# Kernel optimization log

Hardware: AMD Instinct MI355X
Metric: run time of the kernel (lower is better)

The kernel has to match this reference:

```python
import jax, jax.numpy as jnp
import numpy as np

C = 64
C8 = C // 8
C16 = C // 16


def setup_inputs() -> dict:
    key = jax.random.key(0)
    ks = jax.random.split(key, 11)
    s = lambda fan_in: 1.0 / np.sqrt(fan_in)
    return {
        "x": jax.random.normal(ks[0], (4, C, 64, 64), dtype=jnp.float32),
        # 1x1 convs == per-pixel linear: weight [out, in], bias [out]
        "Wq": jax.random.uniform(ks[1], (C8, C), minval=-s(C), maxval=s(C)),
        "bq": jax.random.uniform(ks[2], (C8,), minval=-s(C), maxval=s(C)),
        "Wk": jax.random.uniform(ks[3], (C8, C), minval=-s(C), maxval=s(C)),
        "bk": jax.random.uniform(ks[4], (C8,), minval=-s(C), maxval=s(C)),
        "Wv": jax.random.uniform(ks[5], (C, C), minval=-s(C), maxval=s(C)),
        "bv": jax.random.uniform(ks[6], (C,), minval=-s(C), maxval=s(C)),
        "W1": jax.random.uniform(ks[7], (C16, C), minval=-s(C), maxval=s(C)),
        "b1": jax.random.uniform(ks[8], (C16,), minval=-s(C), maxval=s(C)),
        "W2": jax.random.uniform(ks[9], (C, C16), minval=-s(C16), maxval=s(C16)),
        "b2": jax.random.uniform(ks[10], (C,), minval=-s(C16), maxval=s(C16)),
    }


def reference(x, Wq, bq, Wk, bk, Wv, bv, W1, b1, W2, b2):
    b, c, h, w = x.shape
    n = h * w
    xf = x.reshape(b, c, n)                                   # [b,c,n]
    Q = jnp.einsum('qc,bcn->bnq', Wq, xf) + bq                # [b,n,c/8]
    K = jnp.einsum('kc,bcn->bkn', Wk, xf) + bk[None, :, None] # [b,c/8,n]
    V = jnp.einsum('vc,bcn->bvn', Wv, xf) + bv[None, :, None] # [b,c,n]
    scores = jnp.einsum('bnq,bqm->bnm', Q, K) / jnp.sqrt(jnp.float32(c))
    att = jax.nn.softmax(scores, axis=-1)                     # [b,n,n]
    # self_attention_map = V @ att^T
    sa = jnp.einsum('bvm,bnm->bvn', V, att).reshape(b, c, h, w)
    # SE-style channel gate
    avg = xf.mean(axis=2)                                     # [b,c]
    gate = jax.nn.sigmoid(jax.nn.relu(avg @ W1.T + b1) @ W2.T + b2)
    return sa * gate[:, :, None, None]
```

## Files before the change

kernel.cpp:

```cpp
#include <hip/hip_runtime.h>
#include <hip/hip_bf16.h>

typedef __attribute__((ext_vector_type(8))) short bf16x8;
typedef __attribute__((ext_vector_type(4))) float f32x4;
typedef __attribute__((ext_vector_type(4))) unsigned short u16x4;
typedef __attribute__((ext_vector_type(8))) unsigned short u16x8;

#define WS_QB 0
#define WS_KB 131072
#define WS_VB 262144
#define WS_AVG_U 1310720

__device__ __forceinline__ unsigned short bf_hi(float x) {
    __hip_bfloat16 h = __float2bfloat16(x);
    return *reinterpret_cast<unsigned short*>(&h);
}

__global__ __launch_bounds__(256) void proj_kernel(
    const float* __restrict__ x,
    const float* __restrict__ Wq, const float* __restrict__ bq,
    const float* __restrict__ Wk, const float* __restrict__ bk,
    const float* __restrict__ Wv, const float* __restrict__ bv,
    unsigned short* __restrict__ Qb, unsigned short* __restrict__ Kb,
    unsigned short* __restrict__ Vb, float* __restrict__ avg)
{
    __shared__ __align__(16) unsigned short Wls[80 * 72];

    const int t = threadIdx.x;
    const int w = t >> 6;
    const int l = t & 63;
    const int g = l >> 4;
    const int l15 = l & 15;
    const int b = blockIdx.x >> 6;
    const int n0 = (blockIdx.x & 63) << 6;
    const int n = n0 + w * 16 + l15;
    const float* xb = x + b * 262144;

    float xr[2][8];
#pragma unroll
    for (int kcb = 0; kcb < 2; ++kcb)
#pragma unroll
        for (int j = 0; j < 8; ++j)
            xr[kcb][j] = xb[(kcb * 32 + g * 8 + j) * 4096 + n];

#pragma unroll
    for (int i = 0; i < 20; ++i) {
        const int idx = i * 256 + t;
        const int row = idx >> 6, col = idx & 63;
        float wv;
        if (row < 8)       wv = Wq[row * 64 + col];
        else if (row < 16) wv = Wk[(row - 8) * 64 + col];
        else               wv = Wv[(row - 16) * 64 + col];
        Wls[row * 72 + col] = bf_hi(wv);
    }
    __syncthreads();

    bf16x8 bfr[2];
#pragma unroll
    for (int kcb = 0; kcb < 2; ++kcb)
#pragma unroll
        for (int j = 0; j < 8; ++j)
            bfr[kcb][j] = (short)bf_hi(xr[kcb][j]);

#pragma unroll
    for (int tile = 0; tile < 5; ++tile) {
        const bf16x8 a0 = *(const bf16x8*)&Wls[(tile * 16 + l15) * 72 + g * 8];
        const bf16x8 a1 = *(const bf16x8*)&Wls[(tile * 16 + l15) * 72 + 32 + g * 8];
        f32x4 acc;
#pragma unroll
        for (int r = 0; r < 4; ++r) acc[r] = 0.0f;
        acc = __builtin_amdgcn_mfma_f32_16x16x32_bf16(a0, bfr[0], acc, 0, 0, 0);
        acc = __builtin_amdgcn_mfma_f32_16x16x32_bf16(a1, bfr[1], acc, 0, 0, 0);

        if (tile == 0) {
            u16x4 ov;
            if (g < 2) {
#pragma unroll
                for (int r = 0; r < 4; ++r) ov[r] = bf_hi((acc[r] + bq[g * 4 + r]) * 0.125f);
                *(u16x4*)&Qb[(b * 4096 + n) * 8 + g * 4] = ov;
            } else {
#pragma unroll
                for (int r = 0; r < 4; ++r) ov[r] = bf_hi(acc[r] + bk[(g - 2) * 4 + r]);
                *(u16x4*)&Kb[(b * 4096 + n) * 8 + (g - 2) * 4] = ov;
            }
        } else {
#pragma unroll
            for (int r = 0; r < 4; ++r) {
                const int v = (tile - 1) * 16 + g * 4 + r;
                Vb[(b * 64 + v) * 4096 + n] = bf_hi(acc[r] + bv[v]);
            }
        }
    }

    {
        const int c = t >> 2;
        const float* xrow = xb + c * 4096 + n0 + ((t & 3) << 4);
        float s = 0.0f;
#pragma unroll
        for (int k = 0; k < 4; ++k) {
            const float4 v = *(const float4*)&xrow[k * 4];
            s += (v.x + v.y) + (v.z + v.w);
        }
        s += __shfl_xor(s, 1);
        s += __shfl_xor(s, 2);
        if ((t & 3) == 0) atomicAdd(&avg[b * 64 + c], s * (1.0f / 4096.0f));
    }
}

__global__ __launch_bounds__(256) void attn_kernel(
    const unsigned short* __restrict__ Qb, const unsigned short* __restrict__ Kb,
    const unsigned short* __restrict__ Vb, const float* __restrict__ avg,
    const float* __restrict__ W1, const float* __restrict__ b1,
    const float* __restrict__ W2, const float* __restrict__ b2,
    float* __restrict__ out)
{
    __shared__ __align__(16) unsigned short Vs[2][64][64];
    __shared__ __align__(16) unsigned short Ps[32][64];
    __shared__ float zls[32], gls[64], avgs[64];

    const int t = threadIdx.x;
    const int w = t >> 6;
    const int l = t & 63;
    const int g = l >> 4;
    const int l15 = l & 15;

    const int wg = (blockIdx.x & 7) * 64 + (blockIdx.x >> 3);
    const int b = wg >> 7;
    const int q0 = (wg & 127) << 5;

    if (t < 32) zls[t] = 0.0f;
    if (t < 64) avgs[t] = avg[b * 64 + t];

    bf16x8 zf = {};
    bf16x8 qf[2];
#pragma unroll
    for (int qt = 0; qt < 2; ++qt) {
        bf16x8 v = *(const bf16x8*)&Qb[(b * 4096 + q0 + qt * 16 + l15) * 8];
        qf[qt] = (g == 0) ? v : zf;
    }

    const int srow = t >> 2;
    const int scol = (t & 3) << 4;
    const int ssw = (srow & 7) << 3;
    const unsigned short* vsrc = &Vb[(b * 64 + srow) * 4096];

    {
        u16x8 a = *(const u16x8*)&vsrc[scol];
        u16x8 c = *(const u16x8*)&vsrc[scol + 8];
        *(u16x8*)&Vs[0][srow][scol ^ ssw] = a;
        *(u16x8*)&Vs[0][srow][(scol + 8) ^ ssw] = c;
    }
    const int mrow = w * 16 + l15;
    bf16x8 kf_next;
    {
        bf16x8 kv = *(const bf16x8*)&Kb[(b * 4096 + mrow) * 8];
        kf_next = (g == 0) ? kv : zf;
    }

    f32x4 acc[2];
#pragma unroll
    for (int qt = 0; qt < 2; ++qt)
#pragma unroll
        for (int r = 0; r < 4; ++r) acc[qt][r] = 0.0f;
    float zreg[2] = {0.f, 0.f};
    const int vsw = (l15 & 7) << 3;
    const int psw = (l15 & 7) << 3;

    for (int i = 0; i < 64; ++i) {
        __syncthreads();

        const int inx = (i < 63) ? i + 1 : 63;
        u16x8 va = *(const u16x8*)&vsrc[inx * 64 + scol];
        u16x8 vb2 = *(const u16x8*)&vsrc[inx * 64 + scol + 8];

        bf16x8 kf = kf_next;
        {
            bf16x8 kv = *(const bf16x8*)&Kb[(b * 4096 + inx * 64 + mrow) * 8];
            kf_next = (g == 0) ? kv : zf;
        }
        f32x4 dz;
#pragma unroll
        for (int r = 0; r < 4; ++r) dz[r] = 0.0f;
#pragma unroll
        for (int qt = 0; qt < 2; ++qt) {
            f32x4 d = __builtin_amdgcn_mfma_f32_16x16x32_bf16(kf, qf[qt], dz, 0, 0, 0);
            float p[4];
#pragma unroll
            for (int r = 0; r < 4; ++r) p[r] = __expf(d[r]);
            zreg[qt] += (p[0] + p[1]) + (p[2] + p[3]);
            u16x4 pw;
#pragma unroll
            for (int r = 0; r < 4; ++r) pw[r] = bf_hi(p[r]);
            const int q = qt * 16 + l15;
            *(u16x4*)&Ps[q][(w * 16 + g * 4) ^ ((q & 7) << 3)] = pw;
        }

        __syncthreads();

        {
            unsigned short* dst = &Vs[(i + 1) & 1][srow][0];
            *(u16x8*)&dst[scol ^ ssw] = va;
            *(u16x8*)&dst[(scol + 8) ^ ssw] = vb2;
        }

        {
            const unsigned short* vbuf = &Vs[i & 1][w * 16 + l15][0];
#pragma unroll
            for (int kcb = 0; kcb < 2; ++kcb) {
                const int colA = kcb * 32 + g * 8;
                const bf16x8 af = *(const bf16x8*)&vbuf[colA ^ vsw];
#pragma unroll
                for (int qt = 0; qt < 2; ++qt) {
                    const bf16x8 bfr = *(const bf16x8*)&Ps[qt * 16 + l15][colA ^ psw];
                    acc[qt] = __builtin_amdgcn_mfma_f32_16x16x32_bf16(af, bfr, acc[qt], 0, 0, 0);
                }
            }
        }
    }

#pragma unroll
    for (int qt = 0; qt < 2; ++qt) {
        float z = zreg[qt];
        z += __shfl_xor(z, 16);
        z += __shfl_xor(z, 32);
        if (g == 0) atomicAdd(&zls[qt * 16 + l15], z);
    }
    if (t < 64) {
        float hreg[4];
#pragma unroll
        for (int j = 0; j < 4; ++j) {
            float hh = b1[j];
            for (int c = 0; c < 64; ++c) hh += W1[j * 64 + c] * avgs[c];
            hreg[j] = fmaxf(hh, 0.0f);
        }
        float gg = b2[t];
#pragma unroll
        for (int j = 0; j < 4; ++j) gg += W2[t * 4 + j] * hreg[j];
        gls[t] = 1.0f / (1.0f + __expf(-gg));
    }
    __syncthreads();

#pragma unroll
    for (int qt = 0; qt < 2; ++qt) {
        const int q = qt * 16 + l15;
        const float rz = 1.0f / zls[q];
#pragma unroll
        for (int r = 0; r < 4; ++r) {
            const int v = w * 16 + g * 4 + r;
            out[(b * 64 + v) * 4096 + q0 + q] = acc[qt][r] * rz * gls[v];
        }
    }
}

extern "C" void kernel_launch(void* const* d_in, const int* in_sizes, int n_in,
                              void* d_out, int out_size, void* d_ws, size_t ws_size,
                              hipStream_t stream) {
    const float* x  = (const float*)d_in[0];
    const float* Wq = (const float*)d_in[1];
    const float* bq = (const float*)d_in[2];
    const float* Wk = (const float*)d_in[3];
    const float* bk = (const float*)d_in[4];
    const float* Wv = (const float*)d_in[5];
    const float* bv = (const float*)d_in[6];
    const float* W1 = (const float*)d_in[7];
    const float* b1 = (const float*)d_in[8];
    const float* W2 = (const float*)d_in[9];
    const float* b2 = (const float*)d_in[10];

    unsigned short* wsu = (unsigned short*)d_ws;
    unsigned short* Qb = wsu + WS_QB;
    unsigned short* Kb = wsu + WS_KB;
    unsigned short* Vb = wsu + WS_VB;
    float* avg = (float*)(wsu + WS_AVG_U);
    float* out = (float*)d_out;

    hipMemsetAsync(avg, 0, 256 * sizeof(float), stream);
    proj_kernel<<<256, 256, 0, stream>>>(x, Wq, bq, Wk, bk, Wv, bv, Qb, Kb, Vb, avg);
    attn_kernel<<<512, 256, 0, stream>>>(Qb, Kb, Vb, avg, W1, b1, W2, b2, out);
}
```

Measured before the change: 123.2 us.

## Split projection across output tiles and single-barrier double-buffer attention loop

The projection kernel now launches five times as many blocks, each computing one 16-row output tile (Q/K or a V slice). This raises parallelism but reloads x five times. The attention loop double-buffers the P scratch as well as V, which lets it drop one of the two barriers per iteration. It also raises wave priority around the MFMA section with s_setprio.

```diff
diff --git a/kernel.cpp b/kernel.cpp
--- a/kernel.cpp
+++ b/kernel.cpp
@@ -24,15 +24,18 @@
     unsigned short* __restrict__ Qb, unsigned short* __restrict__ Kb,
     unsigned short* __restrict__ Vb, float* __restrict__ avg)
 {
-    __shared__ __align__(16) unsigned short Wls[80 * 72];
-
-    const int t = threadIdx.x;
-    const int w = t >> 6;
-    const int l = t & 63;
+    __shared__ __align__(16) unsigned short Wls[16 * 72];
+
+    const int tid = threadIdx.x;
+    const int w = tid >> 6;
+    const int l = tid & 63;
     const int g = l >> 4;
     const int l15 = l & 15;
-    const int b = blockIdx.x >> 6;
-    const int n0 = (blockIdx.x & 63) << 6;
+
+    const int tile = blockIdx.x >> 8;
+    const int pair = blockIdx.x & 255;
+    const int b = pair >> 6;
+    const int n0 = (pair & 63) << 6;
     const int n = n0 + w * 16 + l15;
     const float* xb = x + b * 262144;
 
@@ -44,13 +47,12 @@
             xr[kcb][j] = xb[(kcb * 32 + g * 8 + j) * 4096 + n];
 
 #pragma unroll
-    for (int i = 0; i < 20; ++i) {
-        const int idx = i * 256 + t;
+    for (int i = 0; i < 4; ++i) {
+        const int idx = i * 256 + tid;
         const int row = idx >> 6, col = idx & 63;
         float wv;
-        if (row < 8)       wv = Wq[row * 64 + col];
-        else if (row < 16) wv = Wk[(row - 8) * 64 + col];
-        else               wv = Wv[(row - 16) * 64 + col];
+        if (tile == 0) wv = (row < 8) ? Wq[row * 64 + col] : Wk[(row - 8) * 64 + col];
+        else           wv = Wv[((tile - 1) * 16 + row) * 64 + col];
         Wls[row * 72 + col] = bf_hi(wv);
     }
     __syncthreads();
@@ -62,39 +64,27 @@
         for (int j = 0; j < 8; ++j)
             bfr[kcb][j] = (short)bf_hi(xr[kcb][j]);
 
-#pragma unroll
-    for (int tile = 0; tile < 5; ++tile) {
-        const bf16x8 a0 = *(const bf16x8*)&Wls[(tile * 16 + l15) * 72 + g * 8];
-        const bf16x8 a1 = *(const bf16x8*)&Wls[(tile * 16 + l15) * 72 + 32 + g * 8];
-        f32x4 acc;
-#pragma unroll
-        for (int r = 0; r < 4; ++r) acc[r] = 0.0f;
-        acc = __builtin_amdgcn_mfma_f32_16x16x32_bf16(a0, bfr[0], acc, 0, 0, 0);
-        acc = __builtin_amdgcn_mfma_f32_16x16x32_bf16(a1, bfr[1], acc, 0, 0, 0);
-
-        if (tile == 0) {
-            u16x4 ov;
-            if (g < 2) {
-#pragma unroll
-                for (int r = 0; r < 4; ++r) ov[r] = bf_hi((acc[r] + bq[g * 4 + r]) * 0.125f);
-                *(u16x4*)&Qb[(b * 4096 + n) * 8 + g * 4] = ov;
-            } else {
-#pragma unroll
-                for (int r = 0; r < 4; ++r) ov[r] = bf_hi(acc[r] + bk[(g - 2) * 4 + r]);
-                *(u16x4*)&Kb[(b * 4096 + n) * 8 + (g - 2) * 4] = ov;
-            }
+    const bf16x8 a0 = *(const bf16x8*)&Wls[l15 * 72 + g * 8];
+    const bf16x8 a1 = *(const bf16x8*)&Wls[l15 * 72 + 32 + g * 8];
+    f32x4 acc;
+#pragma unroll
+    for (int r = 0; r < 4; ++r) acc[r] = 0.0f;
+    acc = __builtin_amdgcn_mfma_f32_16x16x32_bf16(a0, bfr[0], acc, 0, 0, 0);
+    acc = __builtin_amdgcn_mfma_f32_16x16x32_bf16(a1, bfr[1], acc, 0, 0, 0);
+
+    if (tile == 0) {
+        u16x4 ov;
+        if (g < 2) {
+#pragma unroll
+            for (int r = 0; r < 4; ++r) ov[r] = bf_hi((acc[r] + bq[g * 4 + r]) * 0.125f);
+            *(u16x4*)&Qb[(b * 4096 + n) * 8 + g * 4] = ov;
         } else {
 #pragma unroll
-            for (int r = 0; r < 4; ++r) {
-                const int v = (tile - 1) * 16 + g * 4 + r;
-                Vb[(b * 64 + v) * 4096 + n] = bf_hi(acc[r] + bv[v]);
-            }
-        }
-    }
-
-    {
-        const int c = t >> 2;
-        const float* xrow = xb + c * 4096 + n0 + ((t & 3) << 4);
+            for (int r = 0; r < 4; ++r) ov[r] = bf_hi(acc[r] + bk[(g - 2) * 4 + r]);
+            *(u16x4*)&Kb[(b * 4096 + n) * 8 + (g - 2) * 4] = ov;
+        }
+        const int c = tid >> 2;
+        const float* xrow = xb + c * 4096 + n0 + ((tid & 3) << 4);
         float s = 0.0f;
 #pragma unroll
         for (int k = 0; k < 4; ++k) {
@@ -103,7 +93,13 @@
         }
         s += __shfl_xor(s, 1);
         s += __shfl_xor(s, 2);
-        if ((t & 3) == 0) atomicAdd(&avg[b * 64 + c], s * (1.0f / 4096.0f));
+        if ((tid & 3) == 0) atomicAdd(&avg[b * 64 + c], s * (1.0f / 4096.0f));
+    } else {
+#pragma unroll
+        for (int r = 0; r < 4; ++r) {
+            const int v = (tile - 1) * 16 + g * 4 + r;
+            Vb[(b * 64 + v) * 4096 + n] = bf_hi(acc[r] + bv[v]);
+        }
     }
 }
 
@@ -115,7 +111,7 @@
     float* __restrict__ out)
 {
     __shared__ __align__(16) unsigned short Vs[2][64][64];
-    __shared__ __align__(16) unsigned short Ps[32][64];
+    __shared__ __align__(16) unsigned short Ps[2][32][64];
     __shared__ float zls[32], gls[64], avgs[64];
 
     const int t = threadIdx.x;
@@ -143,18 +139,14 @@
     const int scol = (t & 3) << 4;
     const int ssw = (srow & 7) << 3;
     const unsigned short* vsrc = &Vb[(b * 64 + srow) * 4096];
-
-    {
-        u16x8 a = *(const u16x8*)&vsrc[scol];
-        u16x8 c = *(const u16x8*)&vsrc[scol + 8];
-        *(u16x8*)&Vs[0][srow][scol ^ ssw] = a;
-        *(u16x8*)&Vs[0][srow][(scol + 8) ^ ssw] = c;
-    }
     const int mrow = w * 16 + l15;
-    bf16x8 kf_next;
+
+    u16x8 va = *(const u16x8*)&vsrc[scol];
+    u16x8 vb2 = *(const u16x8*)&vsrc[scol + 8];
+    bf16x8 kreg;
     {
         bf16x8 kv = *(const bf16x8*)&Kb[(b * 4096 + mrow) * 8];
-        kf_next = (g == 0) ? kv : zf;
+        kreg = (g == 0) ? kv : zf;
     }
 
     f32x4 acc[2];
@@ -166,18 +158,26 @@
     const int vsw = (l15 & 7) << 3;
     const int psw = (l15 & 7) << 3;
 
+    __syncthreads();
+
     for (int i = 0; i < 64; ++i) {
-        __syncthreads();
+        const int buf = i & 1;
+
+        {
+            unsigned short* dst = &Vs[buf][srow][0];
+            *(u16x8*)&dst[scol ^ ssw] = va;
+            *(u16x8*)&dst[(scol + 8) ^ ssw] = vb2;
+        }
+        const bf16x8 kf = kreg;
 
         const int inx = (i < 63) ? i + 1 : 63;
-        u16x8 va = *(const u16x8*)&vsrc[inx * 64 + scol];
-        u16x8 vb2 = *(const u16x8*)&vsrc[inx * 64 + scol + 8];
-
-        bf16x8 kf = kf_next;
+        va  = *(const u16x8*)&vsrc[inx * 64 + scol];
+        vb2 = *(const u16x8*)&vsrc[inx * 64 + scol + 8];
         {
             bf16x8 kv = *(const bf16x8*)&Kb[(b * 4096 + inx * 64 + mrow) * 8];
-            kf_next = (g == 0) ? kv : zf;
-        }
+            kreg = (g == 0) ? kv : zf;
+        }
+
         f32x4 dz;
 #pragma unroll
         for (int r = 0; r < 4; ++r) dz[r] = 0.0f;
@@ -192,29 +192,25 @@
 #pragma unroll
             for (int r = 0; r < 4; ++r) pw[r] = bf_hi(p[r]);
             const int q = qt * 16 + l15;
-            *(u16x4*)&Ps[q][(w * 16 + g * 4) ^ ((q & 7) << 3)] = pw;
+            *(u16x4*)&Ps[buf][q][(w * 16 + g * 4) ^ ((q & 7) << 3)] = pw;
         }
 
         __syncthreads();
 
         {
-            unsigned short* dst = &Vs[(i + 1) & 1][srow][0];
-            *(u16x8*)&dst[scol ^ ssw] = va;
-            *(u16x8*)&dst[(scol + 8) ^ ssw] = vb2;
-        }
-
-        {
-            const unsigned short* vbuf = &Vs[i & 1][w * 16 + l15][0];
+            const unsigned short* vbuf = &Vs[buf][w * 16 + l15][0];
+            __builtin_amdgcn_s_setprio(1);
 #pragma unroll
             for (int kcb = 0; kcb < 2; ++kcb) {
                 const int colA = kcb * 32 + g * 8;
                 const bf16x8 af = *(const bf16x8*)&vbuf[colA ^ vsw];
 #pragma unroll
                 for (int qt = 0; qt < 2; ++qt) {
-                    const bf16x8 bfr = *(const bf16x8*)&Ps[qt * 16 + l15][colA ^ psw];
+                    const bf16x8 bfr = *(const bf16x8*)&Ps[buf][qt * 16 + l15][colA ^ psw];
                     acc[qt] = __builtin_amdgcn_mfma_f32_16x16x32_bf16(af, bfr, acc[qt], 0, 0, 0);
                 }
             }
+            __builtin_amdgcn_s_setprio(0);
         }
     }
 
@@ -275,6 +271,6 @@
     float* out = (float*)d_out;
 
     hipMemsetAsync(avg, 0, 256 * sizeof(float), stream);
-    proj_kernel<<<256, 256, 0, stream>>>(x, Wq, bq, Wk, bk, Wv, bv, Qb, Kb, Vb, avg);
+    proj_kernel<<<1280, 256, 0, stream>>>(x, Wq, bq, Wk, bk, Wv, bv, Qb, Kb, Vb, avg);
     attn_kernel<<<512, 256, 0, stream>>>(Qb, Kb, Vb, avg, W1, b1, W2, b2, out);
 }
```

Measured after the change: 114.2 us. 7.3% less time.
